# Kernel optimization log

Hardware: AMD Instinct MI355X
Metric: run time of the kernel (lower is better)

The kernel has to match this reference:

```python
import jax, jax.numpy as jnp
import numpy as np

N = 262144          # number of tracks (batched Python loop)
E = 256             # QD similarity embedding dim
MOTION_DIMS = 7     # observed 3D box dims
STATE_DIMS = 10     # motion_dims + 3 location velocities
MOMENTUM = 0.8      # memory_momentum
INIT_POS_VAR = 10.0     # kf3d_init_mean_cov position variance
INIT_VEL_VAR = 10000.0  # kf3d_init_mean_cov velocity variance


def _kf_mats():
    # constant-velocity transition: x,y,z += vx,vy,vz
    F = jnp.eye(STATE_DIMS, dtype=jnp.float32)
    F = F.at[jnp.arange(3), MOTION_DIMS + jnp.arange(3)].set(1.0)
    Q = jnp.eye(STATE_DIMS, dtype=jnp.float32)      # cov_motion_q
    R = jnp.eye(MOTION_DIMS, dtype=jnp.float32)     # cov_project_r
    return F, Q, R


def setup_inputs() -> dict:
    key = jax.random.key(0)
    ks = jax.random.split(key, 12)
    A = 0.1 * jax.random.normal(ks[4], (N, STATE_DIMS, STATE_DIMS), dtype=jnp.float32)
    prev_covs = jnp.einsum('nij,nkj->nik', A, A) + jnp.eye(STATE_DIMS, dtype=jnp.float32)
    return {
        'boxes_3d': jax.random.normal(ks[0], (N, 12), dtype=jnp.float32),
        'obs_boxes_3d': jax.random.normal(ks[1], (N, MOTION_DIMS), dtype=jnp.float32),
        'prev_boxes7': jax.random.normal(ks[2], (N, MOTION_DIMS), dtype=jnp.float32),
        'prev_means': jax.random.normal(ks[3], (N, STATE_DIMS), dtype=jnp.float32),
        'prev_covs': prev_covs,
        'prev_velocities': jax.random.normal(ks[5], (N, MOTION_DIMS), dtype=jnp.float32),
        'prev_embeddings': jax.random.normal(ks[6], (N, E), dtype=jnp.float32),
        'embeddings': jax.random.normal(ks[7], (N, E), dtype=jnp.float32),
        'acc_frames': jax.random.randint(ks[8], (N,), 0, 10, dtype=jnp.int32),
        'frame_gap': jax.random.randint(ks[9], (N,), 0, 5, dtype=jnp.int32) + 1,
        'matched': jax.random.randint(ks[10], (N,), 0, 2).astype(bool),
        'fps': 2,
    }


def reference(boxes_3d, obs_boxes_3d, prev_boxes7, prev_means, prev_covs,
              prev_velocities, prev_embeddings, embeddings,
              acc_frames, frame_gap, matched, fps):
    F, Q, R = _kf_mats()
    m1 = matched[:, None]

    # ---- matched branch: kf3d_update (H = eye(7,10), so H P H^T = P[:7,:7]) ----
    PHt = prev_covs[:, :, :MOTION_DIMS]                        # P H^T  [N,10,7]
    S = prev_covs[:, :MOTION_DIMS, :MOTION_DIMS] + R           # [N,7,7]
    Kt = jnp.linalg.solve(S, jnp.swapaxes(PHt, 1, 2))          # S^-1 H P  [N,7,10]
    K = jnp.swapaxes(Kt, 1, 2)                                 # [N,10,7]
    innov = obs_boxes_3d - prev_means[:, :MOTION_DIMS]
    mean_u = prev_means + jnp.einsum('nij,nj->ni', K, innov)   # [N,10]
    cov_u = prev_covs - jnp.einsum('nij,njk,nlk->nil', K, S, K)

    # ---- predict location after update (only loc is consumed) ----
    pred_loc = jnp.einsum('ij,nj->ni', F, mean_u)[:, :3]

    # ---- unmatched branch: kf3d_init_mean_cov ----
    mean_i = jnp.concatenate(
        [obs_boxes_3d, jnp.zeros((obs_boxes_3d.shape[0], 3), dtype=obs_boxes_3d.dtype)], axis=1)
    diag_i = jnp.concatenate([jnp.full((MOTION_DIMS,), INIT_POS_VAR, jnp.float32),
                              jnp.full((3,), INIT_VEL_VAR, jnp.float32)])
    cov_i = jnp.diag(diag_i)                                   # [10,10], broadcast in where

    new_means = jnp.where(m1, mean_u, mean_i)
    new_covs = jnp.where(matched[:, None, None], cov_u, cov_i[None])

    # ---- boxes_3d scatter write (matched rows) ----
    pd = mean_u[:, :MOTION_DIMS]
    b_upd = jnp.concatenate(
        [pd[:, :6],                               # cols 0..5
         boxes_3d[:, 6:8],                        # cols 6,7 untouched
         pd[:, 6:7],                              # col 8 = yaw
         (pred_loc - mean_u[:, :3]) * fps],       # cols 9..11 velocity
        axis=1)
    new_boxes_3d = jnp.where(m1, b_upd, boxes_3d)

    # ---- velocity running average ----
    gap = frame_gap.astype(jnp.float32)[:, None]
    acc = acc_frames.astype(jnp.float32)
    vel_obs = (pd - prev_boxes7) / gap
    vel_m = (prev_velocities * acc[:, None] + vel_obs) / (acc[:, None] + 1.0)
    new_velocities = jnp.where(m1, vel_m, jnp.zeros_like(vel_m))
    new_acc_frames = jnp.where(matched, acc + 1.0, jnp.zeros_like(acc))

    # ---- embedding EMA ----
    emb_m = (1.0 - MOMENTUM) * prev_embeddings + MOMENTUM * embeddings
    new_embeddings = jnp.where(m1, emb_m, embeddings)

    return (new_boxes_3d, new_means, new_covs, new_velocities, new_embeddings, new_acc_frames)
```

## Files before the change

### kernel.cpp

```cpp
#include <hip/hip_runtime.h>

__global__ void detect_kernel(const unsigned char* __restrict__ mbytes,
                              int nbytes, int* __restrict__ flag)
{
    int t = threadIdx.x;
    int f = 0;
    for (int i = t; i < nbytes; i += 64)
        if ((i & 3) != 0 && mbytes[i] != 0) f = 1;
    unsigned long long b = __ballot(f != 0);
    if (t == 0) *flag = (b != 0ULL) ? 1 : 0;
}

__device__ __forceinline__ bool get_matched(const void* mptr, int n, int flag)
{
    if (flag) return ((const unsigned char*)mptr)[n] != 0;
    return ((const int*)mptr)[n] != 0;
}

__device__ __forceinline__ float load_scalar_f(const int* p)
{
    int v = *p;
    if (v >= -1000000 && v <= 1000000) return (float)v;
    union { int i; float f; } u; u.i = v; return u.f;
}

__global__ __launch_bounds__(256, 2) void kf_kernel(
    const float* __restrict__ boxes,
    const float* __restrict__ obs,
    const float* __restrict__ pb7,
    const float* __restrict__ pmean,
    const float* __restrict__ pcov,
    const float* __restrict__ pvel,
    const int*   __restrict__ accf,
    const int*   __restrict__ fgap,
    const void*  __restrict__ matched,
    const int*   __restrict__ fps_p,
    const int*   __restrict__ mflag,
    float* __restrict__ oboxes,
    float* __restrict__ omean,
    float* __restrict__ ocov,
    float* __restrict__ ovel,
    float* __restrict__ oacc,
    int N)
{
    int n = blockIdx.x * blockDim.x + threadIdx.x;
    if (n >= N) return;

    const int  flag = *mflag;
    const bool m    = get_matched(matched, n, flag);

    float ob[7];
#pragma unroll
    for (int j = 0; j < 7; j++) ob[j] = obs[(size_t)n * 7 + j];

    if (m) {
        const float fps = load_scalar_f(fps_p);

        float W[10][7], V3[3][3];
        {
            const float4* cp = (const float4*)(pcov + (size_t)n * 100);
#pragma unroll
            for (int i = 0; i < 25; i++) {
                float4 v = cp[i];
                float vv[4] = {v.x, v.y, v.z, v.w};
#pragma unroll
                for (int k = 0; k < 4; k++) {
                    const int e = 4 * i + k, l = e / 10, c = e % 10;
                    if (c < 7)            W[l][c]        = vv[k];
                    else if (l >= 7)      V3[l-7][c-7]   = vv[k];
                }
            }
        }
        float mu[10];
        {
            const float2* mp = (const float2*)(pmean + (size_t)n * 10);
#pragma unroll
            for (int i = 0; i < 5; i++) { float2 v = mp[i]; mu[2*i] = v.x; mu[2*i+1] = v.y; }
        }

        float L[7][7];
#pragma unroll
        for (int k = 0; k < 7; k++) {
            float d = W[k][k] + 1.0f;
#pragma unroll
            for (int q = 0; q < k; q++) d -= L[k][q] * L[k][q];
            float dk = sqrtf(d);
            L[k][k] = dk;
            float inv = 1.0f / dk;
#pragma unroll
            for (int i = k + 1; i < 7; i++) {
                float s = W[i][k];
#pragma unroll
                for (int q = 0; q < k; q++) s -= L[i][q] * L[k][q];
                L[i][k] = s * inv;
            }
        }

        float X[7][10];
#pragma unroll
        for (int j = 0; j < 7; j++) {
            float rinv = 1.0f / L[j][j];
#pragma unroll
            for (int l = 0; l < 10; l++) {
                float s = W[l][j];
#pragma unroll
                for (int q = 0; q < j; q++) s -= L[j][q] * X[q][l];
                X[j][l] = s * rinv;
            }
        }
#pragma unroll
        for (int j = 6; j >= 0; j--) {
            float rinv = 1.0f / L[j][j];
#pragma unroll
            for (int l = 0; l < 10; l++) {
                float s = X[j][l];
#pragma unroll
                for (int q = j + 1; q < 7; q++) s -= L[q][j] * X[q][l];
                X[j][l] = s * rinv;
            }
        }

        float innov[7];
#pragma unroll
        for (int j = 0; j < 7; j++) innov[j] = ob[j] - mu[j];
        float mu_u[10];
#pragma unroll
        for (int l = 0; l < 10; l++) {
            float s = mu[l];
#pragma unroll
            for (int j = 0; j < 7; j++) s += X[j][l] * innov[j];
            mu_u[l] = s;
        }

        {
            float4* op = (float4*)(ocov + (size_t)n * 100);
#pragma unroll
            for (int i = 0; i < 25; i++) {
                float r[4];
#pragma unroll
                for (int k = 0; k < 4; k++) {
                    const int e = 4 * i + k, l = e / 10, c = e % 10;
                    float base = (c < 7) ? W[l][c]
                               : ((l < 7) ? W[c][l] : V3[l-7][c-7]);
                    float s = 0.0f;
#pragma unroll
                    for (int j = 0; j < 7; j++) s += W[l][j] * X[j][c];
                    r[k] = base - s;
                }
                op[i] = make_float4(r[0], r[1], r[2], r[3]);
            }
        }

        float bx6, bx7;
        {
            const float4* bp = (const float4*)(boxes + (size_t)n * 12);
            float4 b = bp[1];
            bx6 = b.z; bx7 = b.w;
        }
        {
            float4* op = (float4*)(oboxes + (size_t)n * 12);
            op[0] = make_float4(mu_u[0], mu_u[1], mu_u[2], mu_u[3]);
            op[1] = make_float4(mu_u[4], mu_u[5], bx6,     bx7);
            op[2] = make_float4(mu_u[6], mu_u[7] * fps, mu_u[8] * fps, mu_u[9] * fps);
        }
        {
            float2* op = (float2*)(omean + (size_t)n * 10);
#pragma unroll
            for (int i = 0; i < 5; i++) op[i] = make_float2(mu_u[2*i], mu_u[2*i+1]);
        }

        float gap  = (float)fgap[n];
        float acc  = (float)accf[n];
        float ginv = 1.0f / gap;
        float ainv = 1.0f / (acc + 1.0f);
#pragma unroll
        for (int j = 0; j < 7; j++) {
            float vobs = (mu_u[j] - pb7[(size_t)n*7 + j]) * ginv;
            ovel[(size_t)n*7 + j] = (pvel[(size_t)n*7 + j] * acc + vobs) * ainv;
        }
        oacc[n] = acc + 1.0f;
    } else {
        {
            const float4* bp = (const float4*)(boxes + (size_t)n * 12);
            float4* op = (float4*)(oboxes + (size_t)n * 12);
            op[0] = bp[0]; op[1] = bp[1]; op[2] = bp[2];
        }
        {
            float2* op = (float2*)(omean + (size_t)n * 10);
            op[0] = make_float2(ob[0], ob[1]);
            op[1] = make_float2(ob[2], ob[3]);
            op[2] = make_float2(ob[4], ob[5]);
            op[3] = make_float2(ob[6], 0.0f);
            op[4] = make_float2(0.0f, 0.0f);
        }
        {
            float4* op = (float4*)(ocov + (size_t)n * 100);
#pragma unroll
            for (int i = 0; i < 25; i++) {
                float r[4];
#pragma unroll
                for (int k = 0; k < 4; k++) {
                    const int e = 4 * i + k, l = e / 10, c = e % 10;
                    r[k] = (l == c) ? ((l < 7) ? 10.0f : 10000.0f) : 0.0f;
                }
                op[i] = make_float4(r[0], r[1], r[2], r[3]);
            }
        }
#pragma unroll
        for (int j = 0; j < 7; j++) ovel[(size_t)n*7 + j] = 0.0f;
        oacc[n] = 0.0f;
    }
}

__global__ __launch_bounds__(256) void emb_kernel(
    const float* __restrict__ pemb,
    const float* __restrict__ emb,
    const void*  __restrict__ matched,
    const int*   __restrict__ mflag,
    float* __restrict__ oemb,
    int N)
{
    int gid  = blockIdx.x * 256 + threadIdx.x;
    int row  = gid >> 6;
    if (row >= N) return;
    int lane = gid & 63;

    const bool m = get_matched(matched, row, *mflag);
    size_t idx = (size_t)row * 64 + lane;

    float4 e = ((const float4*)emb)[idx];
    float4 o;
    if (m) {
        float4 p = ((const float4*)pemb)[idx];
        o.x = 0.2f * p.x + 0.8f * e.x;
        o.y = 0.2f * p.y + 0.8f * e.y;
        o.z = 0.2f * p.z + 0.8f * e.z;
        o.w = 0.2f * p.w + 0.8f * e.w;
    } else {
        o = e;
    }
    ((float4*)oemb)[idx] = o;
}

extern "C" void kernel_launch(void* const* d_in, const int* in_sizes, int n_in,
                              void* d_out, int out_size, void* d_ws, size_t ws_size,
                              hipStream_t stream)
{
    const float* boxes  = (const float*)d_in[0];
    const float* obs    = (const float*)d_in[1];
    const float* pb7    = (const float*)d_in[2];
    const float* pmean  = (const float*)d_in[3];
    const float* pcov   = (const float*)d_in[4];
    const float* pvel   = (const float*)d_in[5];
    const float* pemb   = (const float*)d_in[6];
    const float* emb    = (const float*)d_in[7];
    const int*   accf   = (const int*)d_in[8];
    const int*   fgap   = (const int*)d_in[9];
    const void*  matched= d_in[10];
    const int*   fps_p  = (const int*)d_in[11];
    const int N = in_sizes[8];

    float* out = (float*)d_out;
    float* oboxes = out;
    float* omean  = out + (size_t)N * 12;
    float* ocov   = out + (size_t)N * 22;
    float* ovel   = out + (size_t)N * 122;
    float* oemb   = out + (size_t)N * 129;
    float* oacc   = out + (size_t)N * 385;

    int* mflag = (int*)d_ws;

    detect_kernel<<<1, 64, 0, stream>>>((const unsigned char*)matched, 1024, mflag);
    kf_kernel<<<(N + 255) / 256, 256, 0, stream>>>(
        boxes, obs, pb7, pmean, pcov, pvel, accf, fgap, matched, fps_p, mflag,
        oboxes, omean, ocov, ovel, oacc, N);
    emb_kernel<<<(N + 3) / 4, 256, 0, stream>>>(pemb, emb, matched, mflag, oemb, N);
}
```

Before: 854.6 us.

## Fuse detect, Kalman filter and embedding EMA kernels into one launch

Merges the three kernels into a single launch. Blocks below KFB run the Kalman-filter path and later blocks handle the embedding EMA. Every wave now works out the matched-dtype flag inline with a uint4 load and a ballot, which removes the separate detect kernel and the workspace round-trip. Each embedding wave now handles two rows, and the prev_embeddings load is skipped for unmatched rows. This removes two launches and the serialization between them, so the memory-bound embedding pass can overlap with the KF pass. The cost is a redundant 1 KB flag read in every wave, and if N is too small, fewer than 1 KB of the matched buffer may exist and the flag load could read past it.

```diff
diff --git a/kernel.cpp b/kernel.cpp
--- a/kernel.cpp
+++ b/kernel.cpp
@@ -1,15 +1,5 @@
 #include <hip/hip_runtime.h>
 
-__global__ void detect_kernel(const unsigned char* __restrict__ mbytes,
-                              int nbytes, int* __restrict__ flag)
-{
-    int t = threadIdx.x;
-    int f = 0;
-    for (int i = t; i < nbytes; i += 64)
-        if ((i & 3) != 0 && mbytes[i] != 0) f = 1;
-    unsigned long long b = __ballot(f != 0);
-    if (t == 0) *flag = (b != 0ULL) ? 1 : 0;
-}
 
 __device__ __forceinline__ bool get_matched(const void* mptr, int n, int flag)
 {
@@ -24,30 +14,78 @@
     union { int i; float f; } u; u.i = v; return u.f;
 }
 
-__global__ __launch_bounds__(256, 2) void kf_kernel(
+__global__ __launch_bounds__(256, 2) void fused_kernel(
     const float* __restrict__ boxes,
     const float* __restrict__ obs,
     const float* __restrict__ pb7,
     const float* __restrict__ pmean,
     const float* __restrict__ pcov,
     const float* __restrict__ pvel,
+    const float* __restrict__ pemb,
+    const float* __restrict__ emb,
     const int*   __restrict__ accf,
     const int*   __restrict__ fgap,
     const void*  __restrict__ matched,
     const int*   __restrict__ fps_p,
-    const int*   __restrict__ mflag,
     float* __restrict__ oboxes,
     float* __restrict__ omean,
     float* __restrict__ ocov,
     float* __restrict__ ovel,
+    float* __restrict__ oemb,
     float* __restrict__ oacc,
-    int N)
-{
-    int n = blockIdx.x * blockDim.x + threadIdx.x;
+    int N, int KFB)
+{
+    const int lane = threadIdx.x & 63;
+
+    const uint4 mv = ((const uint4*)matched)[lane];
+    const unsigned bad = (mv.x | mv.y | mv.z | mv.w) & 0xFFFFFF00u;
+    const int flag = (__ballot(bad != 0u) != 0ULL) ? 1 : 0;
+
+    if ((int)blockIdx.x >= KFB) {
+        const int wid  = ((int)blockIdx.x - KFB) * 4 + ((int)threadIdx.x >> 6);
+        const int row0 = wid * 2;
+        if (row0 >= N) return;
+        const bool have1 = (row0 + 1) < N;
+        const size_t idx0 = (size_t)row0 * 64 + lane;
+
+        const bool m0 = get_matched(matched, row0, flag);
+        const bool m1 = have1 && get_matched(matched, row0 + 1, flag);
+
+        const float4* e4 = (const float4*)emb;
+        const float4* p4 = (const float4*)pemb;
+
+        float4 e0 = e4[idx0];
+        float4 e1;
+        if (have1) e1 = e4[idx0 + 64];
+        float4 p0, p1;
+        if (m0) p0 = p4[idx0];
+        if (m1) p1 = p4[idx0 + 64];
+
+        float4 o0 = e0;
+        if (m0) {
+            o0.x = 0.2f * p0.x + 0.8f * e0.x;
+            o0.y = 0.2f * p0.y + 0.8f * e0.y;
+            o0.z = 0.2f * p0.z + 0.8f * e0.z;
+            o0.w = 0.2f * p0.w + 0.8f * e0.w;
+        }
+        ((float4*)oemb)[idx0] = o0;
+        if (have1) {
+            float4 o1 = e1;
+            if (m1) {
+                o1.x = 0.2f * p1.x + 0.8f * e1.x;
+                o1.y = 0.2f * p1.y + 0.8f * e1.y;
+                o1.z = 0.2f * p1.z + 0.8f * e1.z;
+                o1.w = 0.2f * p1.w + 0.8f * e1.w;
+            }
+            ((float4*)oemb)[idx0 + 64] = o1;
+        }
+        return;
+    }
+
+    const int n = (int)blockIdx.x * 256 + (int)threadIdx.x;
     if (n >= N) return;
 
-    const int  flag = *mflag;
-    const bool m    = get_matched(matched, n, flag);
+    const bool m = get_matched(matched, n, flag);
 
     float ob[7];
 #pragma unroll
@@ -210,36 +248,6 @@
         for (int j = 0; j < 7; j++) ovel[(size_t)n*7 + j] = 0.0f;
         oacc[n] = 0.0f;
     }
-}
-
-__global__ __launch_bounds__(256) void emb_kernel(
-    const float* __restrict__ pemb,
-    const float* __restrict__ emb,
-    const void*  __restrict__ matched,
-    const int*   __restrict__ mflag,
-    float* __restrict__ oemb,
-    int N)
-{
-    int gid  = blockIdx.x * 256 + threadIdx.x;
-    int row  = gid >> 6;
-    if (row >= N) return;
-    int lane = gid & 63;
-
-    const bool m = get_matched(matched, row, *mflag);
-    size_t idx = (size_t)row * 64 + lane;
-
-    float4 e = ((const float4*)emb)[idx];
-    float4 o;
-    if (m) {
-        float4 p = ((const float4*)pemb)[idx];
-        o.x = 0.2f * p.x + 0.8f * e.x;
-        o.y = 0.2f * p.y + 0.8f * e.y;
-        o.z = 0.2f * p.z + 0.8f * e.z;
-        o.w = 0.2f * p.w + 0.8f * e.w;
-    } else {
-        o = e;
-    }
-    ((float4*)oemb)[idx] = o;
 }
 
 extern "C" void kernel_launch(void* const* d_in, const int* in_sizes, int n_in,
@@ -268,11 +276,9 @@
     float* oemb   = out + (size_t)N * 129;
     float* oacc   = out + (size_t)N * 385;
 
-    int* mflag = (int*)d_ws;
-
-    detect_kernel<<<1, 64, 0, stream>>>((const unsigned char*)matched, 1024, mflag);
-    kf_kernel<<<(N + 255) / 256, 256, 0, stream>>>(
-        boxes, obs, pb7, pmean, pcov, pvel, accf, fgap, matched, fps_p, mflag,
-        oboxes, omean, ocov, ovel, oacc, N);
-    emb_kernel<<<(N + 3) / 4, 256, 0, stream>>>(pemb, emb, matched, mflag, oemb, N);
-}
+    const int KFB = (N + 255) / 256;
+    const int EMB = (N + 7) / 8;
+    fused_kernel<<<KFB + EMB, 256, 0, stream>>>(
+        boxes, obs, pb7, pmean, pcov, pvel, pemb, emb, accf, fgap, matched,
+        fps_p, oboxes, omean, ocov, ovel, oemb, oacc, N, KFB);
+}
```

Result: slower. 889.3 us (+4.1%).
